# Performance work log

Hardware: AMD Instinct MI355X
Metric: run time of the kernel (lower is better)

## Reference

```python
import jax, jax.numpy as jnp
import numpy as np

JITTER_EPS = 0.01  # router_jitter_noise


def sparsemixer_top2(scores, jitter_eps):
    # scores: [T, E]. Faithful port of PhiMoE sparsemixer (top_k == 2).
    E = scores.shape[-1]
    eye = jnp.arange(E)
    # ---- expert 1 ----
    max1 = jnp.max(scores, axis=-1, keepdims=True)
    ind1 = jnp.argmax(scores, axis=-1)                      # [T]
    factor1 = jnp.maximum(jnp.abs(scores), max1)            # scores.abs().clamp(min=max)
    mask1 = (max1 - scores) / factor1 > 2.0 * jitter_eps
    gates1 = jax.nn.softmax(jnp.where(mask1, -jnp.inf, scores), axis=-1)
    mult1 = jnp.take_along_axis(gates1, ind1[:, None], axis=-1)   # [T,1]
    # ---- expert 2: mask out first pick, repeat ----
    oh1 = eye[None, :] == ind1[:, None]
    masked_scores = jnp.where(oh1, -jnp.inf, scores)
    max2 = jnp.max(masked_scores, axis=-1, keepdims=True)
    ind2 = jnp.argmax(masked_scores, axis=-1)
    factor2 = jnp.maximum(jnp.abs(scores), max2)
    mask2 = (max2 - scores) / factor2 > 2.0 * jitter_eps
    gates2 = jax.nn.softmax(jnp.where(mask2, -jnp.inf, masked_scores), axis=-1)
    mult2 = jnp.take_along_axis(gates2, ind2[:, None], axis=-1)   # [T,1]
    topk_w = jnp.concatenate([mult1, mult2], axis=-1)       # [T,2]
    topk_ids = jnp.stack([ind1, ind2], axis=-1)             # [T,2]
    return topk_w, topk_ids


def setup_inputs() -> dict:
    key = jax.random.key(0)
    ks = jax.random.split(key, 5)
    B, S, D, F, E = 2, 2048, 1024, 2048, 8
    hidden_states = jax.random.normal(ks[0], (B, S, D), dtype=jnp.float32)
    gate_w = jax.random.normal(ks[1], (E, D), dtype=jnp.float32) * (D ** -0.5)
    w_gate = jax.random.normal(ks[2], (E, F, D), dtype=jnp.float32) * (D ** -0.5)
    w_up = jax.random.normal(ks[3], (E, F, D), dtype=jnp.float32) * (D ** -0.5)
    w_down = jax.random.normal(ks[4], (E, D, F), dtype=jnp.float32) * (F ** -0.5)
    return {"hidden_states": hidden_states, "gate_w": gate_w,
            "w_gate": w_gate, "w_up": w_up, "w_down": w_down}


def reference(hidden_states, gate_w, w_gate, w_up, w_down):
    B, S, D = hidden_states.shape
    E = gate_w.shape[0]
    x = hidden_states.reshape(-1, D)                         # [T,D]
    router_logits = x @ gate_w.T                             # [T,E]
    topk_w, topk_ids = sparsemixer_top2(router_logits, JITTER_EPS)
    # per-token combine weights over experts: [T,E]
    comb = jnp.sum(topk_w[:, :, None] *
                   (topk_ids[:, :, None] == jnp.arange(E)[None, None, :]).astype(topk_w.dtype),
                   axis=1)
    out = jnp.zeros_like(x)
    for e in range(E):  # small fixed expert count
        h = jax.nn.silu(x @ w_gate[e].T) * (x @ w_up[e].T)   # [T,F]
        out = out + comb[:, e:e + 1] * (h @ w_down[e].T)     # [T,D]
    return out.reshape(B, S, D), router_logits
```

## Files before the change

### kernel.cpp

```cpp
#include <hip/hip_runtime.h>
#include <stdint.h>

#define TOK    4096
#define DMODEL 1024
#define FDIM   2048
#define NEXP   8
#define MAXP   10240
#define MAXT   40
#define OUT_MAIN (TOK * DMODEL)

#define IDX_NT  24
#define IDX_TE  32
#define IDX_TR  112

#define OFF_META 0
#define OFF_TKW  33792
#define OFF_PTOK 66560
#define OFF_PW   107520
#define OFF_XG   148480
#define OFF_H    21120000
#define OFF_WGB  63063040
#define OFF_WUB  96617472
#define OFF_WDB  130171904
#define OFF_PV   OFF_WGB
#define OFF_RPOS 163726336
#define WS_NEED  163759104

typedef __attribute__((ext_vector_type(8)))  __bf16 bf16x8;
typedef __attribute__((ext_vector_type(8)))  unsigned short u16x8;
typedef __attribute__((ext_vector_type(4)))  unsigned short u16x4;
typedef __attribute__((ext_vector_type(16))) float f32x16;

__device__ __forceinline__ unsigned short f2bf(float f) {
  unsigned u = __builtin_bit_cast(unsigned, f);
  u += 0x7fffu + ((u >> 16) & 1u);
  return (unsigned short)(u >> 16);
}

__device__ __forceinline__ void async_load16(const void* g, void* l) {
  __builtin_amdgcn_global_load_lds(
      (__attribute__((address_space(1))) void*)g,
      (__attribute__((address_space(3))) void*)l, 16, 0, 0);
}

__device__ __forceinline__ bf16x8 ld_frag(const unsigned short* p) {
  return __builtin_bit_cast(bf16x8, *(const u16x8*)p);
}

__global__ void k_prep(const float* __restrict__ wg, const float* __restrict__ wu,
                       const float* __restrict__ wd, unsigned short* __restrict__ wgb,
                       unsigned short* __restrict__ wub, unsigned short* __restrict__ wdb,
                       const float* __restrict__ x, const float* __restrict__ gw,
                       float* __restrict__ logits, int pre) {
  int b = blockIdx.x;
  if (b < 24576) {
    if (!pre) return;
    const float* src; unsigned short* dst; int bb;
    if (b < 8192)       { src = wg; dst = wgb; bb = b; }
    else if (b < 16384) { src = wu; dst = wub; bb = b - 8192; }
    else                { src = wd; dst = wdb; bb = b - 16384; }
    size_t i = ((size_t)bb * 256 + threadIdx.x) * 8;
    float4 a = *(const float4*)(src + i);
    float4 c = *(const float4*)(src + i + 4);
    u16x8 v = {f2bf(a.x), f2bf(a.y), f2bf(a.z), f2bf(a.w),
               f2bf(c.x), f2bf(c.y), f2bf(c.z), f2bf(c.w)};
    *(u16x8*)(dst + i) = v;
    return;
  }
  int lane = threadIdx.x & 63;
  int t = (b - 24576) * 4 + (threadIdx.x >> 6);
  double acc[NEXP];
#pragma unroll
  for (int e = 0; e < NEXP; ++e) acc[e] = 0.0;
  const float* xp = x + (size_t)t * DMODEL;
  for (int i = 0; i < DMODEL / 64; ++i) {
    int d = i * 64 + lane;
    float xv = xp[d];
#pragma unroll
    for (int e = 0; e < NEXP; ++e) acc[e] += (double)xv * (double)gw[e * DMODEL + d];
  }
#pragma unroll
  for (int e = 0; e < NEXP; ++e) {
    double v = acc[e];
#pragma unroll
    for (int off = 32; off > 0; off >>= 1) v += __shfl_down(v, off, 64);
    if (lane == 0) logits[t * NEXP + e] = (float)v;
  }
}

__global__ __launch_bounds__(1024) void k_route2(
    const float* __restrict__ logits, int* __restrict__ meta,
    float* __restrict__ tk_w, int* __restrict__ ptok, float* __restrict__ pw,
    int* __restrict__ rpos) {
  __shared__ int cnt[NEXP], cur[NEXP], seg[NEXP];
  int tid = threadIdx.x;
  if (tid < NEXP) { cnt[tid] = 0; cur[tid] = 0; }
  for (int r = tid; r < MAXP; r += 1024) ptok[r] = -1;
  __syncthreads();
  int i1[4], i2[4]; float w1v[4], w2v[4];
#pragma unroll
  for (int j = 0; j < 4; ++j) {
    int t = tid + j * 1024;
    float s[NEXP];
#pragma unroll
    for (int e = 0; e < NEXP; ++e) s[e] = logits[t * NEXP + e];
    float max1 = s[0]; int ind1 = 0;
#pragma unroll
    for (int e = 1; e < NEXP; ++e) if (s[e] > max1) { max1 = s[e]; ind1 = e; }
    float sum1 = 0.f;
#pragma unroll
    for (int e = 0; e < NEXP; ++e) {
      float f = fmaxf(fabsf(s[e]), max1);
      if (!((max1 - s[e]) / f > 0.02f)) sum1 += expf(s[e] - max1);
    }
    float max2 = -3.4e38f; int ind2 = 0;
#pragma unroll
    for (int e = 0; e < NEXP; ++e) if (e != ind1 && s[e] > max2) { max2 = s[e]; ind2 = e; }
    float sum2 = 0.f;
#pragma unroll
    for (int e = 0; e < NEXP; ++e) {
      if (e == ind1) continue;
      float f = fmaxf(fabsf(s[e]), max2);
      if (!((max2 - s[e]) / f > 0.02f)) sum2 += expf(s[e] - max2);
    }
    i1[j] = ind1; i2[j] = ind2; w1v[j] = 1.f / sum1; w2v[j] = 1.f / sum2;
    atomicAdd(&cnt[ind1], 1);
    atomicAdd(&cnt[ind2], 1);
  }
  __syncthreads();
  if (tid == 0) {
    int off = 0, nt2 = 0;
    for (int e = 0; e < NEXP; ++e) {
      seg[e] = off;
      int tiles = (cnt[e] + 255) >> 8;
      for (int j = 0; j < tiles; ++j) {
        meta[IDX_TE + nt2] = e;
        meta[IDX_TR + nt2] = off + (j << 8);
        ++nt2;
      }
      off += tiles << 8;
    }
    meta[IDX_NT] = nt2;
  }
  __syncthreads();
#pragma unroll
  for (int j = 0; j < 4; ++j) {
    int t = tid + j * 1024;
    int e1 = i1[j];
    int p1 = atomicAdd(&cur[e1], 1);
    int r1 = seg[e1] + p1;
    ptok[r1] = t; pw[r1] = w1v[j]; rpos[2 * t] = r1; tk_w[2 * t] = w1v[j];
    int e2 = i2[j];
    int p2 = atomicAdd(&cur[e2], 1);
    int r2 = seg[e2] + p2;
    ptok[r2] = t; pw[r2] = w2v[j]; rpos[2 * t + 1] = r2; tk_w[2 * t + 1] = w2v[j];
  }
}

__global__ void k_gather(const float* __restrict__ x, const int* __restrict__ ptok,
                         unsigned short* __restrict__ xg) {
  int r = blockIdx.x;
  int t = ptok[r];
  int c = threadIdx.x << 2;
  unsigned short o0 = 0, o1 = 0, o2 = 0, o3 = 0;
  if (t >= 0) {
    float4 v = *(const float4*)(x + ((size_t)t << 10) + c);
    o0 = f2bf(v.x); o1 = f2bf(v.y); o2 = f2bf(v.z); o3 = f2bf(v.w);
  }
  u16x4 o = {o0, o1, o2, o3};
  *(u16x4*)(xg + ((size_t)r << 10) + c) = o;
}

template <bool PRE>
__global__ __launch_bounds__(512, 2) void k_gu(
    const unsigned short* __restrict__ xg,
    const float* __restrict__ wg32, const float* __restrict__ wu32,
    const unsigned short* __restrict__ wgb, const unsigned short* __restrict__ wub,
    unsigned short* __restrict__ h, const int* __restrict__ meta) {
  int nt = meta[IDX_NT];
  int rt = blockIdx.y;
  if (rt >= nt) return;
  int e = meta[IDX_TE + rt];
  int row0 = meta[IDX_TR + rt];
  int n0 = blockIdx.x * 128;

  __shared__ __align__(16) unsigned short sA[2][16384];
  __shared__ __align__(16) unsigned short sBg[2][8192];
  __shared__ __align__(16) unsigned short sBu[2][8192];

  int tid = threadIdx.x, lane = tid & 63, w = tid >> 6;
  int wm = w & 1, wn = w >> 1;
  int l31 = lane & 31, lh = lane >> 5;

  f32x16 accg[4], accu[4];
#pragma unroll
  for (int m = 0; m < 4; ++m) {
#pragma unroll
    for (int r = 0; r < 16; ++r) { accg[m][r] = 0.f; accu[m][r] = 0.f; }
  }

  const unsigned short* Abase =
      xg + (size_t)(row0 + w * 32 + l31) * DMODEL + lh * 8;
  int cb0 = w * 2, cb1 = cb0 + 1;
  const unsigned short *G0, *G1, *U0, *U1;
  if constexpr (PRE) {
    const unsigned short* WgB = wgb + (size_t)e * FDIM * DMODEL;
    const unsigned short* WuB = wub + (size_t)e * FDIM * DMODEL;
    size_t o0 = (size_t)(n0 + ((cb0 >> 2) << 5) + l31) * DMODEL + ((cb0 & 3) << 4) + lh * 8;
    size_t o1 = (size_t)(n0 + ((cb1 >> 2) << 5) + l31) * DMODEL + ((cb1 & 3) << 4) + lh * 8;
    G0 = WgB + o0; G1 = WgB + o1; U0 = WuB + o0; U1 = WuB + o1;
  }
  const float* Wg = nullptr; const float* Wu = nullptr;
  if constexpr (!PRE) {
    Wg = wg32 + (size_t)e * FDIM * DMODEL;
    Wu = wu32 + (size_t)e * FDIM * DMODEL;
  }

  auto stage = [&](int buf, int ks) {
    int k0 = ks * 64;
    async_load16(Abase + k0,      &sA[buf][(w * 4 + 0) * 512]);
    async_load16(Abase + k0 + 16, &sA[buf][(w * 4 + 1) * 512]);
    async_load16(Abase + k0 + 32, &sA[buf][(w * 4 + 2) * 512]);
    async_load16(Abase + k0 + 48, &sA[buf][(w * 4 + 3) * 512]);
    if constexpr (PRE) {
      async_load16(G0 + k0, &sBg[buf][cb0 * 512]);
      async_load16(G1 + k0, &sBg[buf][cb1 * 512]);
      async_load16(U0 + k0, &sBu[buf][cb0 * 512]);
      async_load16(U1 + k0, &sBu[buf][cb1 * 512]);
    } else {
#pragma unroll
      for (int i2 = 0; i2 < 2; ++i2) {
        int tau = tid + 512 * i2;
        int c = tau >> 6, l = tau & 63;
        int nrow = n0 + ((c >> 2) << 5) + (l & 31);
        int kk = k0 + ((c & 3) << 4) + ((l >> 5) << 3);
        const float* sg = Wg + (size_t)nrow * DMODEL + kk;
        const float* su = Wu + (size_t)nrow * DMODEL + kk;
        float4 g0 = *(const float4*)sg;
        float4 g1 = *(const float4*)(sg + 4);
        float4 u0 = *(const float4*)su;
        float4 u1 = *(const float4*)(su + 4);
        u16x8 vg = {f2bf(g0.x), f2bf(g0.y), f2bf(g0.z), f2bf(g0.w),
                    f2bf(g1.x), f2bf(g1.y), f2bf(g1.z), f2bf(g1.w)};
        u16x8 vu = {f2bf(u0.x), f2bf(u0.y), f2bf(u0.z), f2bf(u0.w),
                    f2bf(u1.x), f2bf(u1.y), f2bf(u1.z), f2bf(u1.w)};
        *(u16x8*)&sBg[buf][c * 512 + l * 8] = vg;
        *(u16x8*)&sBu[buf][c * 512 + l * 8] = vu;
      }
    }
  };

  auto compute = [&](int buf) {
#pragma unroll
    for (int kq = 0; kq < 4; ++kq) {
      bf16x8 a0 = ld_frag(&sA[buf][((wm * 4 + 0) * 4 + kq) * 512 + lane * 8]);
      bf16x8 a1 = ld_frag(&sA[buf][((wm * 4 + 1) * 4 + kq) * 512 + lane * 8]);
      bf16x8 a2 = ld_frag(&sA[buf][((wm * 4 + 2) * 4 + kq) * 512 + lane * 8]);
      bf16x8 a3 = ld_frag(&sA[buf][((wm * 4 + 3) * 4 + kq) * 512 + lane * 8]);
      bf16x8 vg = ld_frag(&sBg[buf][(wn * 4 + kq) * 512 + lane * 8]);
      bf16x8 vu = ld_frag(&sBu[buf][(wn * 4 + kq) * 512 + lane * 8]);
      accg[0] = __builtin_amdgcn_mfma_f32_32x32x16_bf16(a0, vg, accg[0], 0, 0, 0);
      accg[1] = __builtin_amdgcn_mfma_f32_32x32x16_bf16(a1, vg, accg[1], 0, 0, 0);
      accg[2] = __builtin_amdgcn_mfma_f32_32x32x16_bf16(a2, vg, accg[2], 0, 0, 0);
      accg[3] = __builtin_amdgcn_mfma_f32_32x32x16_bf16(a3, vg, accg[3], 0, 0, 0);
      accu[0] = __builtin_amdgcn_mfma_f32_32x32x16_bf16(a0, vu, accu[0], 0, 0, 0);
      accu[1] = __builtin_amdgcn_mfma_f32_32x32x16_bf16(a1, vu, accu[1], 0, 0, 0);
      accu[2] = __builtin_amdgcn_mfma_f32_32x32x16_bf16(a2, vu, accu[2], 0, 0, 0);
      accu[3] = __builtin_amdgcn_mfma_f32_32x32x16_bf16(a3, vu, accu[3], 0, 0, 0);
    }
  };

  stage(0, 0);
  __syncthreads();
  int cur = 0;
  for (int ks = 0; ks < DMODEL / 64; ++ks) {
    if (ks + 1 < DMODEL / 64) stage(cur ^ 1, ks + 1);
    compute(cur);
    __syncthreads();
    cur ^= 1;
  }

  int col = n0 + wn * 32 + l31;
#pragma unroll
  for (int m = 0; m < 4; ++m) {
#pragma unroll
    for (int r = 0; r < 16; ++r) {
      int lrow = wm * 128 + m * 32 + (r & 3) + ((r >> 2) << 3) + lh * 4;
      float gv = accg[m][r], uv = accu[m][r];
      float hv = gv * uv / (1.f + __expf(-gv));
      h[(size_t)(row0 + lrow) * FDIM + col] = f2bf(hv);
    }
  }
}

template <bool PRE>
__global__ __launch_bounds__(512, 2) void k_down(
    const unsigned short* __restrict__ h, const float* __restrict__ wd32,
    const unsigned short* __restrict__ wdb, float* __restrict__ out,
    float* __restrict__ pv, const int* __restrict__ meta,
    const int* __restrict__ ptok, const float* __restrict__ pw) {
  int nt = meta[IDX_NT];
  int rt = blockIdx.y;
  if (rt >= nt) return;
  int e = meta[IDX_TE + rt];
  int row0 = meta[IDX_TR + rt];
  int d0 = blockIdx.x * 128;

  __shared__ __align__(16) unsigned short sA[2][16384];
  __shared__ __align__(16) unsigned short sB[2][8192];
  __shared__ int stok[256];
  __shared__ float sw_[256];

  int tid = threadIdx.x, lane = tid & 63, w = tid >> 6;
  int wm = w & 1, wn = w >> 1;
  int l31 = lane & 31, lh = lane >> 5;

  if constexpr (!PRE) {
    if (tid < 256) { stok[tid] = ptok[row0 + tid]; sw_[tid] = pw[row0 + tid]; }
  }

  f32x16 acc[4];
#pragma unroll
  for (int m = 0; m < 4; ++m) {
#pragma unroll
    for (int r = 0; r < 16; ++r) acc[m][r] = 0.f;
  }

  const unsigned short* Abase =
      h + (size_t)(row0 + w * 32 + l31) * FDIM + lh * 8;
  int cb0 = w * 2, cb1 = cb0 + 1;
  const unsigned short *D0, *D1;
  if constexpr (PRE) {
    const unsigned short* WdB = wdb + (size_t)e * DMODEL * FDIM;
    D0 = WdB + (size_t)(d0 + ((cb0 >> 2) << 5) + l31) * FDIM + ((cb0 & 3) << 4) + lh * 8;
    D1 = WdB + (size_t)(d0 + ((cb1 >> 2) << 5) + l31) * FDIM + ((cb1 & 3) << 4) + lh * 8;
  }
  const float* Wd = nullptr;
  if constexpr (!PRE) Wd = wd32 + (size_t)e * DMODEL * FDIM;

  auto stage = [&](int buf, int ks) {
    int k0 = ks * 64;
    async_load16(Abase + k0,      &sA[buf][(w * 4 + 0) * 512]);
    async_load16(Abase + k0 + 16, &sA[buf][(w * 4 + 1) * 512]);
    async_load16(Abase + k0 + 32, &sA[buf][(w * 4 + 2) * 512]);
    async_load16(Abase + k0 + 48, &sA[buf][(w * 4 + 3) * 512]);
    if constexpr (PRE) {
      async_load16(D0 + k0, &sB[buf][cb0 * 512]);
      async_load16(D1 + k0, &sB[buf][cb1 * 512]);
    } else {
#pragma unroll
      for (int i2 = 0; i2 < 2; ++i2) {
        int tau = tid + 512 * i2;
        int c = tau >> 6, l = tau & 63;
        int drow = d0 + ((c >> 2) << 5) + (l & 31);
        int kk = k0 + ((c & 3) << 4) + ((l >> 5) << 3);
        const float* sd = Wd + (size_t)drow * FDIM + kk;
        float4 b0 = *(const float4*)sd;
        float4 b1 = *(const float4*)(sd + 4);
        u16x8 vb = {f2bf(b0.x), f2bf(b0.y), f2bf(b0.z), f2bf(b0.w),
                    f2bf(b1.x), f2bf(b1.y), f2bf(b1.z), f2bf(b1.w)};
        *(u16x8*)&sB[buf][c * 512 + l * 8] = vb;
      }
    }
  };

  auto compute = [&](int buf) {
#pragma unroll
    for (int kq = 0; kq < 4; ++kq) {
      bf16x8 a0 = ld_frag(&sA[buf][((wm * 4 + 0) * 4 + kq) * 512 + lane * 8]);
      bf16x8 a1 = ld_frag(&sA[buf][((wm * 4 + 1) * 4 + kq) * 512 + lane * 8]);
      bf16x8 a2 = ld_frag(&sA[buf][((wm * 4 + 2) * 4 + kq) * 512 + lane * 8]);
      bf16x8 a3 = ld_frag(&sA[buf][((wm * 4 + 3) * 4 + kq) * 512 + lane * 8]);
      bf16x8 vb = ld_frag(&sB[buf][(wn * 4 + kq) * 512 + lane * 8]);
      acc[0] = __builtin_amdgcn_mfma_f32_32x32x16_bf16(a0, vb, acc[0], 0, 0, 0);
      acc[1] = __builtin_amdgcn_mfma_f32_32x32x16_bf16(a1, vb, acc[1], 0, 0, 0);
      acc[2] = __builtin_amdgcn_mfma_f32_32x32x16_bf16(a2, vb, acc[2], 0, 0, 0);
      acc[3] = __builtin_amdgcn_mfma_f32_32x32x16_bf16(a3, vb, acc[3], 0, 0, 0);
    }
  };

  stage(0, 0);
  __syncthreads();
  int cur = 0;
  for (int ks = 0; ks < FDIM / 64; ++ks) {
    if (ks + 1 < FDIM / 64) stage(cur ^ 1, ks + 1);
    compute(cur);
    __syncthreads();
    cur ^= 1;
  }

  int col = d0 + wn * 32 + l31;
#pragma unroll
  for (int m = 0; m < 4; ++m) {
#pragma unroll
    for (int r = 0; r < 16; ++r) {
      int lrow = wm * 128 + m * 32 + (r & 3) + ((r >> 2) << 3) + lh * 4;
      if constexpr (PRE) {
        pv[(size_t)(row0 + lrow) * DMODEL + col] = acc[m][r];
      } else {
        int t = stok[lrow];
        if (t >= 0) atomicAdd(&out[(size_t)t * DMODEL + col], acc[m][r] * sw_[lrow]);
      }
    }
  }
}

__global__ void k_combine(const float* __restrict__ pv, const int* __restrict__ rpos,
                          const float* __restrict__ tkw, float* __restrict__ out) {
  int t = blockIdx.x;
  int r1 = rpos[2 * t], r2 = rpos[2 * t + 1];
  float w1 = tkw[2 * t], w2 = tkw[2 * t + 1];
  int c = threadIdx.x << 2;
  float4 a = *(const float4*)(pv + (size_t)r1 * DMODEL + c);
  float4 b = *(const float4*)(pv + (size_t)r2 * DMODEL + c);
  float4 o;
  o.x = w1 * a.x + w2 * b.x;
  o.y = w1 * a.y + w2 * b.y;
  o.z = w1 * a.z + w2 * b.z;
  o.w = w1 * a.w + w2 * b.w;
  *(float4*)(out + (size_t)t * DMODEL + c) = o;
}

extern "C" void kernel_launch(void* const* d_in, const int* in_sizes, int n_in,
                              void* d_out, int out_size, void* d_ws, size_t ws_size,
                              hipStream_t stream) {
  const float* x  = (const float*)d_in[0];
  const float* gw = (const float*)d_in[1];
  const float* wg = (const float*)d_in[2];
  const float* wu = (const float*)d_in[3];
  const float* wd = (const float*)d_in[4];
  float* out = (float*)d_out;
  float* logits = out + OUT_MAIN;

  char* wsb = (char*)d_ws;
  int* meta = (int*)(wsb + OFF_META);
  float* tk_w = (float*)(wsb + OFF_TKW);
  int* ptok = (int*)(wsb + OFF_PTOK);
  float* pw = (float*)(wsb + OFF_PW);
  unsigned short* xg = (unsigned short*)(wsb + OFF_XG);
  unsigned short* h = (unsigned short*)(wsb + OFF_H);
  unsigned short* wgb = (unsigned short*)(wsb + OFF_WGB);
  unsigned short* wub = (unsigned short*)(wsb + OFF_WUB);
  unsigned short* wdb = (unsigned short*)(wsb + OFF_WDB);
  float* pv = (float*)(wsb + OFF_PV);
  int* rpos = (int*)(wsb + OFF_RPOS);

  bool pre = ws_size >= (size_t)WS_NEED;
  if (!pre) hipMemsetAsync(out, 0, (size_t)OUT_MAIN * sizeof(float), stream);

  k_prep<<<25600, 256, 0, stream>>>(wg, wu, wd, wgb, wub, wdb, x, gw, logits, (int)pre);
  k_route2<<<1, 1024, 0, stream>>>(logits, meta, tk_w, ptok, pw, rpos);
  k_gather<<<MAXP, 256, 0, stream>>>(x, ptok, xg);
  if (pre) {
    k_gu<true><<<dim3(FDIM / 128, MAXT), 512, 0, stream>>>(xg, wg, wu, wgb, wub, h, meta);
    k_down<true><<<dim3(DMODEL / 128, MAXT), 512, 0, stream>>>(h, wd, wdb, out, pv, meta, ptok, pw);
    k_combine<<<TOK, 256, 0, stream>>>(pv, rpos, tk_w, out);
  } else {
    k_gu<false><<<dim3(FDIM / 128, MAXT), 512, 0, stream>>>(xg, wg, wu, wgb, wub, h, meta);
    k_down<false><<<dim3(DMODEL / 128, MAXT), 512, 0, stream>>>(h, wd, wdb, out, pv, meta, ptok, pw);
  }
}
```

Baseline: 559.0 us.

## Use partial vmcnt waits and setprio in pre-staged gate/up and down GEMM loops

For the PRE template path of both GEMM kernels, the full __syncthreads after each stage is replaced by a partial s_waitcnt vmcnt that waits only for the previous stage's loads, plus raw s_barrier calls. The MFMA compute block is wrapped in s_setprio(1)/s_setprio(0) and the loop is unrolled by 2. The goal is to keep the next tile's global loads in flight while the current tile computes and to favour MFMA-issuing waves. This relies on the stage lambda issuing exactly the assumed number of loads, using direct-to-LDS or otherwise vmcnt-tracked loads; if the count is wrong there is a race.

```diff
diff --git a/kernel.cpp b/kernel.cpp
--- a/kernel.cpp
+++ b/kernel.cpp
@@ -270,14 +270,32 @@
     }
   };
 
+  int cur = 0;
   stage(0, 0);
-  __syncthreads();
-  int cur = 0;
-  for (int ks = 0; ks < DMODEL / 64; ++ks) {
-    if (ks + 1 < DMODEL / 64) stage(cur ^ 1, ks + 1);
-    compute(cur);
+  if constexpr (PRE) {
+#pragma unroll 2
+    for (int ks = 0; ks < DMODEL / 64; ++ks) {
+      if (ks + 1 < DMODEL / 64) {
+        stage(cur ^ 1, ks + 1);
+        asm volatile("s_waitcnt vmcnt(8)" ::: "memory");
+      } else {
+        asm volatile("s_waitcnt vmcnt(0)" ::: "memory");
+      }
+      __builtin_amdgcn_s_barrier();
+      __builtin_amdgcn_s_setprio(1);
+      compute(cur);
+      __builtin_amdgcn_s_setprio(0);
+      __builtin_amdgcn_s_barrier();
+      cur ^= 1;
+    }
+  } else {
     __syncthreads();
-    cur ^= 1;
+    for (int ks = 0; ks < DMODEL / 64; ++ks) {
+      if (ks + 1 < DMODEL / 64) stage(cur ^ 1, ks + 1);
+      compute(cur);
+      __syncthreads();
+      cur ^= 1;
+    }
   }
 
   int col = n0 + wn * 32 + l31;
@@ -379,14 +397,32 @@
     }
   };
 
+  int cur = 0;
   stage(0, 0);
-  __syncthreads();
-  int cur = 0;
-  for (int ks = 0; ks < FDIM / 64; ++ks) {
-    if (ks + 1 < FDIM / 64) stage(cur ^ 1, ks + 1);
-    compute(cur);
+  if constexpr (PRE) {
+#pragma unroll 2
+    for (int ks = 0; ks < FDIM / 64; ++ks) {
+      if (ks + 1 < FDIM / 64) {
+        stage(cur ^ 1, ks + 1);
+        asm volatile("s_waitcnt vmcnt(6)" ::: "memory");
+      } else {
+        asm volatile("s_waitcnt vmcnt(0)" ::: "memory");
+      }
+      __builtin_amdgcn_s_barrier();
+      __builtin_amdgcn_s_setprio(1);
+      compute(cur);
+      __builtin_amdgcn_s_setprio(0);
+      __builtin_amdgcn_s_barrier();
+      cur ^= 1;
+    }
+  } else {
     __syncthreads();
-    cur ^= 1;
+    for (int ks = 0; ks < FDIM / 64; ++ks) {
+      if (ks + 1 < FDIM / 64) stage(cur ^ 1, ks + 1);
+      compute(cur);
+      __syncthreads();
+      cur ^= 1;
+    }
   }
 
   int col = d0 + wn * 32 + l31;
```

Result: faster. 537.6 us (-3.8%).
